# Optimization experiments

Hardware: AMD Instinct MI355X
Metric: run time of the kernel (lower is better)

The kernel has to match this reference:

```python
import jax, jax.numpy as jnp
import numpy as np

N_CAT, IN, HID, VOCAB, B = 512, 1536, 2048, 32000, 256
C = N_CAT + IN + HID  # cell_size = 4096


def setup_inputs() -> dict:
    key = jax.random.key(0)
    ks = jax.random.split(key, 16)
    s = 1.0 / np.sqrt(C)
    inp = {
        "category": jax.random.normal(ks[0], (B, N_CAT), jnp.float32),
        "x": jax.random.normal(ks[1], (B, IN), jnp.float32),
        "hidden": jax.random.normal(ks[2], (B, HID), jnp.float32),
        "cell": jnp.zeros((B, C), jnp.float32),
        # gate weights, torch Linear layout [out, in]
        "Wf": jax.random.uniform(ks[3], (C, C), jnp.float32, -s, s),
        "bf": jax.random.uniform(ks[4], (C,), jnp.float32, -s, s),
        "Wi": jax.random.uniform(ks[5], (C, C), jnp.float32, -s, s),
        "bi": jax.random.uniform(ks[6], (C,), jnp.float32, -s, s),
        "Wc": jax.random.uniform(ks[7], (C, C), jnp.float32, -s, s),
        "bc": jax.random.uniform(ks[8], (C,), jnp.float32, -s, s),
        "Wo": jax.random.uniform(ks[9], (C, C), jnp.float32, -s, s),
        "bo": jax.random.uniform(ks[10], (C,), jnp.float32, -s, s),
        "Wout": jax.random.uniform(ks[11], (VOCAB, C), jnp.float32, -s, s),
        "bout": jax.random.uniform(ks[12], (VOCAB,), jnp.float32, -s, s),
    }
    return inp


def reference(category, x, hidden, cell, Wf, bf, Wi, bi, Wc, bc, Wo, bo, Wout, bout):
    # concat inputs: [B, C]
    xc = jnp.concatenate([category, x, hidden], axis=1)
    # fuse the 4 gate linears into one GEMM: [B, 4C]
    Wall = jnp.concatenate([Wf, Wi, Wc, Wo], axis=0)   # [4C, C]
    ball = jnp.concatenate([bf, bi, bc, bo], axis=0)   # [4C]
    z = xc @ Wall.T + ball
    f, i, g, o = jnp.split(z, 4, axis=1)
    f = jax.nn.sigmoid(f)
    i = jax.nn.sigmoid(i)
    g = jnp.tanh(g)
    o = jax.nn.sigmoid(o)
    cell_new = f * cell + i * g                        # [B, C]
    hidden_new = o * jnp.tanh(cell_new)                # [B, C]
    out = hidden_new @ Wout.T + bout                   # [B, VOCAB]
    # dropout is identity in eval mode
    out = jax.nn.log_softmax(out, axis=1)
    return (out, cell_new, hidden_new)
```

## Files before the change

kernel.cpp:

```cpp
#include <hip/hip_runtime.h>
#include <cmath>

typedef __bf16 bf16x8 __attribute__((ext_vector_type(8)));
typedef float  f32x4  __attribute__((ext_vector_type(4)));

#define ATILE 32768
#define LDS_W_OFF 65536
#define WTILE 8192

#define GLOAD_LDS16(g, l)                                                    \
    __builtin_amdgcn_global_load_lds(                                        \
        (const __attribute__((address_space(1))) unsigned int*)(g),          \
        (__attribute__((address_space(3))) unsigned int*)(l), 16, 0, 0)

__device__ __forceinline__ int swz(int row, int byteInRow) {
    return row * 128 + (byteInRow ^ ((row & 7) << 4));
}

__device__ __forceinline__ bf16x8 cvt8(f32x4 a, f32x4 b) {
    bf16x8 r;
    r[0] = (__bf16)a[0]; r[1] = (__bf16)a[1]; r[2] = (__bf16)a[2]; r[3] = (__bf16)a[3];
    r[4] = (__bf16)b[0]; r[5] = (__bf16)b[1]; r[6] = (__bf16)b[2]; r[7] = (__bf16)b[3];
    return r;
}

__global__ __launch_bounds__(256)
void prep_xc(const float* __restrict__ cat, const float* __restrict__ x,
             const float* __restrict__ hid, unsigned char* __restrict__ A0)
{
    int id  = blockIdx.x * 256 + threadIdx.x;
    int row = id >> 9, col = (id & 511) * 8;
    const float* src = (col < 512)  ? cat + (size_t)row * 512 + col
                     : (col < 2048) ? x   + (size_t)row * 1536 + (col - 512)
                                    : hid + (size_t)row * 2048 + (col - 2048);
    f32x4 a = *(const f32x4*)src, b = *(const f32x4*)(src + 4);
    int ks = col >> 6, c8 = (col & 63) >> 3;
    *(bf16x8*)(A0 + (size_t)ks * ATILE + swz(row, c8 * 16)) = cvt8(a, b);
}

template <int MODE>
__global__ __launch_bounds__(512, 4)
void gemm_bf16(const unsigned char* __restrict__ At,
               const float* __restrict__ W0, const float* __restrict__ W1,
               const float* __restrict__ W2, const float* __restrict__ W3,
               const float* __restrict__ B0, const float* __restrict__ B1,
               const float* __restrict__ B2, const float* __restrict__ B3,
               float* __restrict__ out, int ldout)
{
    __shared__ __align__(16) unsigned char lds[2 * ATILE + 2 * WTILE];

    const int tid  = threadIdx.x;
    const int lane = tid & 63;
    const int wid  = tid >> 6;
    const int l15  = lane & 15;
    const int l4   = lane >> 4;
    const int wr   = wid >> 1;
    const int wc   = wid & 1;

    int n0, koff, nk; float* outp;
    if (MODE == 0) {
        n0 = (blockIdx.x >> 1) * 64;
        int kh = blockIdx.x & 1;
        koff = kh * 32; nk = 32;
        outp = out + (size_t)kh * 4194304;
    } else {
        n0 = blockIdx.x * 64; koff = 0; nk = 64; outp = out;
    }

    const float* Wsrc; const float* Bsrc; int wn0;
    if (MODE == 0) {
        int g = n0 >> 12;
        Wsrc = (g == 0) ? W0 : (g == 1) ? W1 : (g == 2) ? W2 : W3;
        Bsrc = (g == 0) ? B0 : (g == 1) ? B1 : (g == 2) ? B2 : B3;
        wn0  = n0 & 4095;
    } else {
        Wsrc = W0; Bsrc = B0; wn0 = n0;
    }

    f32x4 wreg[2][2];
    f32x4 acc[4][2] = {};

    const int wrow = tid >> 3, wc8 = tid & 7;
    const float* wbase = Wsrc + (size_t)(wn0 + wrow) * 4096 + wc8 * 8;

    auto issueA = [&](int ks, int buf) {
        const unsigned char* src = At + (size_t)(koff + ks) * ATILE + wid * 4096 + lane * 16;
        unsigned char* dst = lds + buf * ATILE + wid * 4096;
        #pragma unroll
        for (int i = 0; i < 4; ++i)
            GLOAD_LDS16(src + i * 1024, dst + i * 1024);
    };
    auto loadW = [&](int ks, int slot) {
        const float* p = wbase + (size_t)(koff + ks) * 64;
        wreg[slot][0] = *(const f32x4*)p;
        wreg[slot][1] = *(const f32x4*)(p + 4);
    };
    auto storeW = [&](int slot, int buf) {
        *(bf16x8*)(lds + LDS_W_OFF + buf * WTILE + swz(wrow, wc8 * 16)) =
            cvt8(wreg[slot][0], wreg[slot][1]);
    };

    issueA(0, 0); loadW(0, 0);
    issueA(1, 1); loadW(1, 1);
    asm volatile("s_waitcnt vmcnt(6)" ::: "memory");
    __builtin_amdgcn_sched_barrier(0);
    storeW(0, 0);
    asm volatile("s_waitcnt lgkmcnt(0)" ::: "memory");
    __builtin_amdgcn_s_barrier();

    for (int t = 0; t < nk; ++t) {
        const int cur = t & 1;
        unsigned char* abase = lds + cur * ATILE;
        unsigned char* wlds  = lds + LDS_W_OFF + cur * WTILE;

        bf16x8 af[2][4], bw[2][2];
        #pragma unroll
        for (int kk = 0; kk < 2; ++kk) {
            #pragma unroll
            for (int m = 0; m < 4; ++m) {
                int row = wr * 64 + m * 16 + l15;
                af[kk][m] = *(const bf16x8*)(abase + swz(row, kk * 64 + l4 * 16));
            }
            #pragma unroll
            for (int n = 0; n < 2; ++n) {
                int row = wc * 32 + n * 16 + l15;
                bw[kk][n] = *(const bf16x8*)(wlds + swz(row, kk * 64 + l4 * 16));
            }
        }
        asm volatile("s_waitcnt lgkmcnt(0)" ::: "memory");
        __builtin_amdgcn_sched_barrier(0);
        __builtin_amdgcn_s_barrier();
        __builtin_amdgcn_sched_barrier(0);

        if (t + 2 < nk) { issueA(t + 2, cur); loadW(t + 2, cur); }
        #pragma unroll
        for (int kk = 0; kk < 2; ++kk)
            #pragma unroll
            for (int m = 0; m < 4; ++m)
                #pragma unroll
                for (int n = 0; n < 2; ++n)
                    acc[m][n] = __builtin_amdgcn_mfma_f32_16x16x32_bf16(
                        af[kk][m], bw[kk][n], acc[m][n], 0, 0, 0);
        if (t + 1 < nk) {
            if (t + 2 < nk) asm volatile("s_waitcnt vmcnt(6)" ::: "memory");
            else            asm volatile("s_waitcnt vmcnt(0)" ::: "memory");
            __builtin_amdgcn_sched_barrier(0);
            storeW(cur ^ 1, cur ^ 1);
            asm volatile("s_waitcnt lgkmcnt(0)" ::: "memory");
        }
        __builtin_amdgcn_s_barrier();
        __builtin_amdgcn_sched_barrier(0);
    }

    #pragma unroll
    for (int n = 0; n < 2; ++n) {
        int col = wc * 32 + n * 16 + l15;
        float bias = (MODE == 1 || koff == 0) ? Bsrc[wn0 + col] : 0.0f;
        #pragma unroll
        for (int m = 0; m < 4; ++m) {
            int row = wr * 64 + m * 16 + l4 * 4;
            f32x4 v = acc[m][n];
            #pragma unroll
            for (int j = 0; j < 4; ++j)
                outp[(size_t)(row + j) * ldout + n0 + col] = v[j] + bias;
        }
    }
}

__global__ __launch_bounds__(256)
void lstm_elem(const float* __restrict__ z0, const float* __restrict__ z1,
               const float* __restrict__ cell,
               float* __restrict__ cnew, float* __restrict__ hnew,
               unsigned char* __restrict__ A1)
{
    int id  = blockIdx.x * 256 + threadIdx.x;
    int row = id >> 9, col = (id & 511) * 8;
    const float* za = z0 + (size_t)row * 16384 + col;
    const float* zb = z1 + (size_t)row * 16384 + col;
    f32x4 vf[2], vi[2], vg[2], vo[2];
    #pragma unroll
    for (int h = 0; h < 2; ++h) {
        vf[h] = *(const f32x4*)(za + h * 4)         + *(const f32x4*)(zb + h * 4);
        vi[h] = *(const f32x4*)(za + 4096 + h * 4)  + *(const f32x4*)(zb + 4096 + h * 4);
        vg[h] = *(const f32x4*)(za + 8192 + h * 4)  + *(const f32x4*)(zb + 8192 + h * 4);
        vo[h] = *(const f32x4*)(za + 12288 + h * 4) + *(const f32x4*)(zb + 12288 + h * 4);
    }
    const float* cr = cell + (size_t)row * 4096 + col;
    f32x4 vc[2] = { *(const f32x4*)cr, *(const f32x4*)(cr + 4) };
    f32x4 rc[2], rh[2];
    bf16x8 hb;
    #pragma unroll
    for (int h = 0; h < 2; ++h)
        #pragma unroll
        for (int j = 0; j < 4; ++j) {
            float f = 1.0f / (1.0f + __expf(-vf[h][j]));
            float i = 1.0f / (1.0f + __expf(-vi[h][j]));
            float g = tanhf(vg[h][j]);
            float o = 1.0f / (1.0f + __expf(-vo[h][j]));
            float cn = f * vc[h][j] + i * g;
            float hn = o * tanhf(cn);
            rc[h][j] = cn; rh[h][j] = hn;
            hb[h * 4 + j] = (__bf16)hn;
        }
    float* cd = cnew + (size_t)row * 4096 + col;
    float* hd = hnew + (size_t)row * 4096 + col;
    *(f32x4*)cd = rc[0]; *(f32x4*)(cd + 4) = rc[1];
    *(f32x4*)hd = rh[0]; *(f32x4*)(hd + 4) = rh[1];
    int ks = col >> 6, c8 = (col & 63) >> 3;
    *(bf16x8*)(A1 + (size_t)ks * ATILE + swz(row, c8 * 16)) = hb;
}

__global__ __launch_bounds__(256)
void logsoftmax_inplace(float* __restrict__ out)
{
    float* row    = out + (size_t)blockIdx.x * 32000;
    const int tid = threadIdx.x;
    __shared__ float redm[4], reds[4];

    float m = -1e30f, s = 0.0f;
    for (int i = tid; i < 8000; i += 256) {
        f32x4 v = *(const f32x4*)(row + i * 4);
        float t = fmaxf(fmaxf(v[0], v[1]), fmaxf(v[2], v[3]));
        float nm = fmaxf(m, t);
        s = s * __expf(m - nm) + __expf(v[0] - nm) + __expf(v[1] - nm)
                               + __expf(v[2] - nm) + __expf(v[3] - nm);
        m = nm;
    }
    #pragma unroll
    for (int off = 32; off; off >>= 1) {
        float om = __shfl_xor(m, off), os = __shfl_xor(s, off);
        float nm = fmaxf(m, om);
        s = s * __expf(m - nm) + os * __expf(om - nm);
        m = nm;
    }
    if ((tid & 63) == 0) { redm[tid >> 6] = m; reds[tid >> 6] = s; }
    __syncthreads();
    {
        float M = fmaxf(fmaxf(redm[0], redm[1]), fmaxf(redm[2], redm[3]));
        float S = reds[0] * __expf(redm[0] - M) + reds[1] * __expf(redm[1] - M)
                + reds[2] * __expf(redm[2] - M) + reds[3] * __expf(redm[3] - M);
        m = M; s = S;
    }
    float lse = m + logf(s);

    for (int i = tid; i < 8000; i += 256) {
        f32x4 v = *(const f32x4*)(row + i * 4);
        v[0] -= lse; v[1] -= lse; v[2] -= lse; v[3] -= lse;
        *(f32x4*)(row + i * 4) = v;
    }
}

extern "C" void kernel_launch(void* const* d_in, const int* in_sizes, int n_in,
                              void* d_out, int out_size, void* d_ws, size_t ws_size,
                              hipStream_t stream)
{
    const float* cat  = (const float*)d_in[0];
    const float* x    = (const float*)d_in[1];
    const float* hid  = (const float*)d_in[2];
    const float* cell = (const float*)d_in[3];
    const float* Wf   = (const float*)d_in[4];
    const float* bf   = (const float*)d_in[5];
    const float* Wi   = (const float*)d_in[6];
    const float* bi   = (const float*)d_in[7];
    const float* Wc   = (const float*)d_in[8];
    const float* bc   = (const float*)d_in[9];
    const float* Wo   = (const float*)d_in[10];
    const float* bo   = (const float*)d_in[11];
    const float* Wout = (const float*)d_in[12];
    const float* bout = (const float*)d_in[13];
    float* out = (float*)d_out;

    unsigned char* A0 = (unsigned char*)d_ws;
    unsigned char* A1 = A0 + (size_t)64 * ATILE;
    float*         z  = (float*)(A1 + (size_t)64 * ATILE);

    float* cnew = out + 8192000;
    float* hnew = out + 9240576;

    prep_xc<<<512, 256, 0, stream>>>(cat, x, hid, A0);
    gemm_bf16<0><<<512, 512, 0, stream>>>(A0, Wf, Wi, Wc, Wo, bf, bi, bc, bo, z, 16384);
    lstm_elem<<<512, 256, 0, stream>>>(z, z + 4194304, cell, cnew, hnew, A1);
    gemm_bf16<1><<<500, 512, 0, stream>>>(A1, Wout, Wout, Wout, Wout,
                                          bout, bout, bout, bout, out, 32000);
    logsoftmax_inplace<<<256, 256, 0, stream>>>(out);
}
```

Before: 287.1 us.

## Widen GEMM N-tile to 128 columns and unroll double-buffer loop

Each GEMM block now computes 128 output columns instead of 64, so every A tile staged in LDS feeds twice as many MFMAs and the grids halve (256 and 250 blocks). The W staging is rewritten so each thread loads and converts 16 floats per k-step, and the k-loop is unrolled by two with compile-time buffer indices to remove runtime buffer selection. In exchange, LDS use and accumulator registers double, the occupancy hint drops from 4 to 2, and with only 250-256 blocks the 256-CU device may be left underfilled.

```diff
diff --git a/kernel.cpp b/kernel.cpp
--- a/kernel.cpp
+++ b/kernel.cpp
@@ -4,9 +4,11 @@
 typedef __bf16 bf16x8 __attribute__((ext_vector_type(8)));
 typedef float  f32x4  __attribute__((ext_vector_type(4)));
 
+template <int N> struct IC { static constexpr int v = N; };
+
 #define ATILE 32768
+#define WTILE 16384
 #define LDS_W_OFF 65536
-#define WTILE 8192
 
 #define GLOAD_LDS16(g, l)                                                    \
     __builtin_amdgcn_global_load_lds(                                        \
@@ -39,7 +41,7 @@
 }
 
 template <int MODE>
-__global__ __launch_bounds__(512, 4)
+__global__ __launch_bounds__(512, 2)
 void gemm_bf16(const unsigned char* __restrict__ At,
                const float* __restrict__ W0, const float* __restrict__ W1,
                const float* __restrict__ W2, const float* __restrict__ W3,
@@ -48,6 +50,8 @@
                float* __restrict__ out, int ldout)
 {
     __shared__ __align__(16) unsigned char lds[2 * ATILE + 2 * WTILE];
+
+    constexpr int NKT = (MODE == 0) ? 32 : 64;
 
     const int tid  = threadIdx.x;
     const int lane = tid & 63;
@@ -57,14 +61,14 @@
     const int wr   = wid >> 1;
     const int wc   = wid & 1;
 
-    int n0, koff, nk; float* outp;
+    int n0, koff; float* outp;
     if (MODE == 0) {
-        n0 = (blockIdx.x >> 1) * 64;
+        n0 = (blockIdx.x >> 1) * 128;
         int kh = blockIdx.x & 1;
-        koff = kh * 32; nk = 32;
+        koff = kh * 32;
         outp = out + (size_t)kh * 4194304;
     } else {
-        n0 = blockIdx.x * 64; koff = 0; nk = 64; outp = out;
+        n0 = blockIdx.x * 128; koff = 0; outp = out;
     }
 
     const float* Wsrc; const float* Bsrc; int wn0;
@@ -77,11 +81,12 @@
         Wsrc = W0; Bsrc = B0; wn0 = n0;
     }
 
-    f32x4 wreg[2][2];
-    f32x4 acc[4][2] = {};
-
-    const int wrow = tid >> 3, wc8 = tid & 7;
-    const float* wbase = Wsrc + (size_t)(wn0 + wrow) * 4096 + wc8 * 8;
+    f32x4 wreg[2][4];
+    f32x4 acc[4][4] = {};
+
+    const int wrow = tid >> 2;
+    const int wkc  = tid & 3;
+    const float* wbase = Wsrc + (size_t)(wn0 + wrow) * 4096 + (size_t)koff * 64 + wkc * 16;
 
     auto issueA = [&](int ks, int buf) {
         const unsigned char* src = At + (size_t)(koff + ks) * ATILE + wid * 4096 + lane * 16;
@@ -90,30 +95,37 @@
         for (int i = 0; i < 4; ++i)
             GLOAD_LDS16(src + i * 1024, dst + i * 1024);
     };
-    auto loadW = [&](int ks, int slot) {
-        const float* p = wbase + (size_t)(koff + ks) * 64;
-        wreg[slot][0] = *(const f32x4*)p;
-        wreg[slot][1] = *(const f32x4*)(p + 4);
+    auto loadW = [&](int ks, auto slot) {
+        constexpr int S = decltype(slot)::v;
+        const float* p = wbase + (size_t)ks * 64;
+        wreg[S][0] = *(const f32x4*)p;
+        wreg[S][1] = *(const f32x4*)(p + 4);
+        wreg[S][2] = *(const f32x4*)(p + 8);
+        wreg[S][3] = *(const f32x4*)(p + 12);
     };
-    auto storeW = [&](int slot, int buf) {
-        *(bf16x8*)(lds + LDS_W_OFF + buf * WTILE + swz(wrow, wc8 * 16)) =
-            cvt8(wreg[slot][0], wreg[slot][1]);
+    auto storeW = [&](auto slot, int buf) {
+        constexpr int S = decltype(slot)::v;
+        unsigned char* b = lds + LDS_W_OFF + buf * WTILE;
+        *(bf16x8*)(b + swz(wrow, wkc * 32))      = cvt8(wreg[S][0], wreg[S][1]);
+        *(bf16x8*)(b + swz(wrow, wkc * 32 + 16)) = cvt8(wreg[S][2], wreg[S][3]);
     };
 
-    issueA(0, 0); loadW(0, 0);
-    issueA(1, 1); loadW(1, 1);
-    asm volatile("s_waitcnt vmcnt(6)" ::: "memory");
+    issueA(0, 0); loadW(0, IC<0>{});
+    issueA(1, 1); loadW(1, IC<1>{});
+    asm volatile("s_waitcnt vmcnt(8)" ::: "memory");
     __builtin_amdgcn_sched_barrier(0);
-    storeW(0, 0);
+    storeW(IC<0>{}, 0);
     asm volatile("s_waitcnt lgkmcnt(0)" ::: "memory");
     __builtin_amdgcn_s_barrier();
-
-    for (int t = 0; t < nk; ++t) {
-        const int cur = t & 1;
-        unsigned char* abase = lds + cur * ATILE;
-        unsigned char* wlds  = lds + LDS_W_OFF + cur * WTILE;
-
-        bf16x8 af[2][4], bw[2][2];
+    __builtin_amdgcn_sched_barrier(0);
+
+    auto step = [&](int t, auto curc) {
+        constexpr int CUR = decltype(curc)::v;
+        constexpr int OTH = CUR ^ 1;
+        unsigned char* abase = lds + CUR * ATILE;
+        unsigned char* wlds  = lds + LDS_W_OFF + CUR * WTILE;
+
+        bf16x8 af[2][4], bw[2][4];
         #pragma unroll
         for (int kk = 0; kk < 2; ++kk) {
             #pragma unroll
@@ -122,8 +134,8 @@
                 af[kk][m] = *(const bf16x8*)(abase + swz(row, kk * 64 + l4 * 16));
             }
             #pragma unroll
-            for (int n = 0; n < 2; ++n) {
-                int row = wc * 32 + n * 16 + l15;
+            for (int n = 0; n < 4; ++n) {
+                int row = wc * 64 + n * 16 + l15;
                 bw[kk][n] = *(const bf16x8*)(wlds + swz(row, kk * 64 + l4 * 16));
             }
         }
@@ -132,29 +144,34 @@
         __builtin_amdgcn_s_barrier();
         __builtin_amdgcn_sched_barrier(0);
 
-        if (t + 2 < nk) { issueA(t + 2, cur); loadW(t + 2, cur); }
+        if (t + 2 < NKT) { issueA(t + 2, CUR); loadW(t + 2, curc); }
         #pragma unroll
         for (int kk = 0; kk < 2; ++kk)
             #pragma unroll
             for (int m = 0; m < 4; ++m)
                 #pragma unroll
-                for (int n = 0; n < 2; ++n)
+                for (int n = 0; n < 4; ++n)
                     acc[m][n] = __builtin_amdgcn_mfma_f32_16x16x32_bf16(
                         af[kk][m], bw[kk][n], acc[m][n], 0, 0, 0);
-        if (t + 1 < nk) {
-            if (t + 2 < nk) asm volatile("s_waitcnt vmcnt(6)" ::: "memory");
-            else            asm volatile("s_waitcnt vmcnt(0)" ::: "memory");
+        if (t + 1 < NKT) {
+            if (t + 2 < NKT) asm volatile("s_waitcnt vmcnt(8)" ::: "memory");
+            else             asm volatile("s_waitcnt vmcnt(0)" ::: "memory");
             __builtin_amdgcn_sched_barrier(0);
-            storeW(cur ^ 1, cur ^ 1);
+            storeW(IC<OTH>{}, OTH);
             asm volatile("s_waitcnt lgkmcnt(0)" ::: "memory");
         }
         __builtin_amdgcn_s_barrier();
         __builtin_amdgcn_sched_barrier(0);
+    };
+
+    for (int t = 0; t < NKT; t += 2) {
+        step(t,     IC<0>{});
+        step(t + 1, IC<1>{});
     }
 
     #pragma unroll
-    for (int n = 0; n < 2; ++n) {
-        int col = wc * 32 + n * 16 + l15;
+    for (int n = 0; n < 4; ++n) {
+        int col = wc * 64 + n * 16 + l15;
         float bias = (MODE == 1 || koff == 0) ? Bsrc[wn0 + col] : 0.0f;
         #pragma unroll
         for (int m = 0; m < 4; ++m) {
@@ -278,9 +295,9 @@
     float* hnew = out + 9240576;
 
     prep_xc<<<512, 256, 0, stream>>>(cat, x, hid, A0);
-    gemm_bf16<0><<<512, 512, 0, stream>>>(A0, Wf, Wi, Wc, Wo, bf, bi, bc, bo, z, 16384);
+    gemm_bf16<0><<<256, 512, 0, stream>>>(A0, Wf, Wi, Wc, Wo, bf, bi, bc, bo, z, 16384);
     lstm_elem<<<512, 256, 0, stream>>>(z, z + 4194304, cell, cnew, hnew, A1);
-    gemm_bf16<1><<<500, 512, 0, stream>>>(A1, Wout, Wout, Wout, Wout,
+    gemm_bf16<1><<<250, 512, 0, stream>>>(A1, Wout, Wout, Wout, Wout,
                                           bout, bout, bout, bout, out, 32000);
     logsoftmax_inplace<<<256, 256, 0, stream>>>(out);
 }
```

New measurement: 276.2 us. -3.8%, faster.
